# Kernel optimization log

Hardware: AMD Instinct MI355X
Metric: run time of the kernel (lower is better)

The kernel has to match this reference:

```python
import jax, jax.numpy as jnp
import numpy as np

B_SCALE = 1.3195079565048218  # per_level_scale
N_LEVELS = 4                  # kernel hardcodes 4 levels
F = 4                         # kernel hardcodes 4 features per level
BASE = 32.0                   # kernel hardcodes base resolution 32
MAX_PARAMS = 2 ** 19
N_POINTS = 2097152


def _level_meta():
    offsets = []
    off = 0
    for i in range(N_LEVELS):
        res = int(np.ceil(BASE * np.exp(i * np.log(B_SCALE)) - 1.0)) + 1
        p = res ** 3
        p = p if p % 8 == 0 else ((p + 7) // 8) * 8
        p = min(MAX_PARAMS, p)
        offsets.append(off)
        off += p
    return offsets, off

OFFSETS, TOTAL_PARAMS = _level_meta()
TOTAL_HASH_SIZE = TOTAL_PARAMS * F  # 2772480


def setup_inputs() -> dict:
    key = jax.random.key(0)
    k1, k2 = jax.random.split(key)
    # scale to [0, 0.9) so all 8 corner indices stay inside each level's grid
    positions = jax.random.uniform(k1, (N_POINTS, 3), dtype=jnp.float32) * 0.9
    # original init: uniform(-1e-4, 1e-4); small random values
    table = jax.random.normal(k2, (TOTAL_HASH_SIZE,), dtype=jnp.float32) * 1e-4
    return {"positions": positions, "table": table}


def _encode(positions, table):
    tab = table.reshape(-1, F)  # [total_params, 4]
    n = positions.shape[0]
    outs = []
    for level in range(N_LEVELS):
        scale = BASE * (B_SCALE ** level) - 1.0
        res = int(np.ceil(scale)) + 1
        pos = positions * scale + 0.5            # [n,3]
        grid = jnp.floor(pos)
        frac = pos - grid                         # trilinear fractions
        grid = grid.astype(jnp.int32)
        acc = jnp.zeros((n, F), positions.dtype)
        for c in range(8):  # 8 corners of the cell
            w = jnp.ones((n,), positions.dtype)
            idx = jnp.zeros((n,), jnp.int32)
            stride = 1
            for d in range(3):
                if (c >> d) & 1:
                    coord = grid[:, d] + 1
                    w = w * frac[:, d]
                else:
                    coord = grid[:, d]
                    w = w * (1.0 - frac[:, d])
                idx = idx + coord * stride
                stride *= res
            acc = acc + w[:, None] * tab[OFFSETS[level] + idx]
        outs.append(acc)
    return jnp.concatenate(outs, axis=1)  # [n, 16]


def reference(positions, table):
    return _encode(positions, table)
```

## Files before the change

kernel.cpp:

```cpp
#include <hip/hip_runtime.h>
#include <math.h>


#define NBINS        512
#define BIN_SCALE    (8.0f / 0.9f)
#define SCAT_THREADS 512
#define PTS_PER_BLK  4096
#define SCAT_ITERS   (PTS_PER_BLK / SCAT_THREADS)
#define CAP          4608

#define ENC_THREADS  512
#define ENC_BPB      (CAP / ENC_THREADS)

#define D1 7
#define D2 9
#define D3 11
#define A1 0
#define A2 (A1 + D1*D1*D1)
#define A3 (A2 + D2*D2*D2)
#define LDS_TOT (A3 + D3*D3*D3)

typedef float vfloat4 __attribute__((ext_vector_type(4)));

__device__ __forceinline__ int bin_of(float x, float y, float z) {
    int bx = (int)(x * BIN_SCALE); bx = bx < 0 ? 0 : (bx > 7 ? 7 : bx);
    int by = (int)(y * BIN_SCALE); by = by < 0 ? 0 : (by > 7 ? 7 : by);
    int bz = (int)(z * BIN_SCALE); bz = bz < 0 ? 0 : (bz > 7 ? 7 : bz);
    return bx | (by << 3) | (bz << 6);
}


__global__ __launch_bounds__(SCAT_THREADS) void scatter_cap_kernel(
    const float* __restrict__ pos, int n, int* __restrict__ cursor,
    float4* __restrict__ sorted, int bin_stride)
{
    __shared__ float4         lds_rec[PTS_PER_BLK];
    __shared__ unsigned short lds_bin[PTS_PER_BLK];
    __shared__ int lds_hist[NBINS];
    __shared__ int lds_lbase[NBINS];
    __shared__ int lds_gbase[NBINS];

    int tid = threadIdx.x;
    long base = (long)blockIdx.x * PTS_PER_BLK;
    lds_hist[tid] = 0;
    __syncthreads();

    float px[SCAT_ITERS], py[SCAT_ITERS], pz[SCAT_ITERS];
    int br[SCAT_ITERS];
#pragma unroll
    for (int j = 0; j < SCAT_ITERS; ++j) {
        long p = base + j * SCAT_THREADS + tid;
        int packed = -1;
        if (p < n) {
            float x = pos[3 * p], y = pos[3 * p + 1], z = pos[3 * p + 2];
            px[j] = x; py[j] = y; pz[j] = z;
            int b = bin_of(x, y, z);
            int r = atomicAdd(&lds_hist[b], 1);
            packed = (r << 9) | b;
        }
        br[j] = packed;
    }
    __syncthreads();

    int cntb = lds_hist[tid];
    lds_lbase[tid] = cntb;
    __syncthreads();
    for (int off = 1; off < NBINS; off <<= 1) {
        int v = (tid >= off) ? lds_lbase[tid - off] : 0;
        __syncthreads();
        lds_lbase[tid] += v;
        __syncthreads();
    }
    int excl = lds_lbase[tid] - cntb;
    if (cntb) lds_gbase[tid] = atomicAdd(&cursor[tid], cntb);
    lds_lbase[tid] = excl;
    __syncthreads();

#pragma unroll
    for (int j = 0; j < SCAT_ITERS; ++j) {
        if (br[j] < 0) continue;
        int b = br[j] & (NBINS - 1);
        int r = br[j] >> 9;
        int s = lds_lbase[b] + r;
        long p = base + j * SCAT_THREADS + tid;
        lds_rec[s] = make_float4(px[j], py[j], pz[j], __int_as_float((int)p));
        lds_bin[s] = (unsigned short)b;
    }
    __syncthreads();

    long rem = (long)n - base;
    int tot = rem >= PTS_PER_BLK ? PTS_PER_BLK : (rem > 0 ? (int)rem : 0);
    for (int s = tid; s < tot; s += SCAT_THREADS) {
        float4 rec = lds_rec[s];
        int b = lds_bin[s];
        int off_in_bin = s - lds_lbase[b];
        long slot = (long)b * bin_stride + lds_gbase[b] + off_in_bin;
        sorted[slot] = rec;
    }
}

template<int D>
__device__ __forceinline__ void stage_win(
    float4* __restrict__ dst, const float4* __restrict__ tab,
    int off, int res, int Bx, int By, int Bz, int tid)
{
    const int DD = D * D, DDD = D * D * D;
    for (int e = tid; e < DDD; e += ENC_THREADS) {
        int iz  = e / DD;
        int rem = e - iz * DD;
        int iy  = rem / D;
        int ix  = rem - iy * D;
        int gx = Bx + ix; gx = gx < 0 ? 0 : (gx > res - 1 ? res - 1 : gx);
        int gy = By + iy; gy = gy < 0 ? 0 : (gy > res - 1 ? res - 1 : gy);
        int gz = Bz + iz; gz = gz < 0 ? 0 : (gz > res - 1 ? res - 1 : gz);
        dst[e] = tab[off + gx + gy * res + gz * res * res];
    }
}

__device__ __forceinline__ float4 interp_global(
    const float4* __restrict__ tab,
    float x, float y, float z, float scale, int res, int off)
{
    float hx = x * scale + 0.5f, hy = y * scale + 0.5f, hz = z * scale + 0.5f;
    float fx = floorf(hx), fy = floorf(hy), fz = floorf(hz);
    float wx = hx - fx, wy = hy - fy, wz = hz - fz;
    float ox = 1.0f - wx, oy = 1.0f - wy, oz = 1.0f - wz;
    int res2  = res * res;
    int basei = off + (int)fx + (int)fy * res + (int)fz * res2;
    float4 acc = make_float4(0.f, 0.f, 0.f, 0.f);
#pragma unroll
    for (int c = 0; c < 8; ++c) {
        int   idx = basei + ((c & 1) ? 1 : 0) + ((c & 2) ? res : 0) + ((c & 4) ? res2 : 0);
        float w   = ((c & 1) ? wx : ox) * ((c & 2) ? wy : oy) * ((c & 4) ? wz : oz);
        float4 v  = tab[idx];
        acc.x += w * v.x; acc.y += w * v.y; acc.z += w * v.z; acc.w += w * v.w;
    }
    return acc;
}

template<int D>
__device__ __forceinline__ float4 interp_one(
    const float4* __restrict__ lds, const float4* __restrict__ tab,
    float x, float y, float z, float scale, int res, int off,
    int Bx, int By, int Bz)
{
    float hx = x * scale + 0.5f, hy = y * scale + 0.5f, hz = z * scale + 0.5f;
    float fx = floorf(hx), fy = floorf(hy), fz = floorf(hz);
    float wx = hx - fx, wy = hy - fy, wz = hz - fz;
    float ox = 1.0f - wx, oy = 1.0f - wy, oz = 1.0f - wz;
    int gx = (int)fx, gy = (int)fy, gz = (int)fz;
    int lx = gx - Bx, ly = gy - By, lz = gz - Bz;
    float4 acc = make_float4(0.f, 0.f, 0.f, 0.f);
    if ((unsigned)lx <= (unsigned)(D - 2) &&
        (unsigned)ly <= (unsigned)(D - 2) &&
        (unsigned)lz <= (unsigned)(D - 2)) {
        int basei = (lz * D + ly) * D + lx;
#pragma unroll
        for (int c = 0; c < 8; ++c) {
            int   idx = basei + ((c & 1) ? 1 : 0) + ((c & 2) ? D : 0) + ((c & 4) ? D * D : 0);
            float w   = ((c & 1) ? wx : ox) * ((c & 2) ? wy : oy) * ((c & 4) ? wz : oz);
            float4 v  = lds[idx];
            acc.x += w * v.x; acc.y += w * v.y; acc.z += w * v.z; acc.w += w * v.w;
        }
    } else {
        int res2  = res * res;
        int basei = off + gx + gy * res + gz * res2;
#pragma unroll
        for (int c = 0; c < 8; ++c) {
            int   idx = basei + ((c & 1) ? 1 : 0) + ((c & 2) ? res : 0) + ((c & 4) ? res2 : 0);
            float w   = ((c & 1) ? wx : ox) * ((c & 2) ? wy : oy) * ((c & 4) ? wz : oz);
            float4 v  = tab[idx];
            acc.x += w * v.x; acc.y += w * v.y; acc.z += w * v.z; acc.w += w * v.w;
        }
    }
    return acc;
}

__global__ __launch_bounds__(ENC_THREADS) void encode_cap_lds_kernel(
    const float4* __restrict__ sorted,
    const int* __restrict__ cursor,
    const float4* __restrict__ tab,
    float4* __restrict__ out,
    float s0, float s1, float s2, float s3,
    int r0, int r1, int r2, int r3,
    int o0, int o1, int o2, int o3)
{
    __shared__ float4 lds[LDS_TOT];

    int nb = (int)gridDim.x;
    int lb = (int)blockIdx.x;
    lb = (lb & 7) * (nb >> 3) + (lb >> 3);

    int b   = lb / ENC_BPB;
    int k   = lb - b * ENC_BPB;
    int cnt = cursor[b];
    if (k * ENC_THREADS >= cnt) return;

    int tid = threadIdx.x;

    int local = k * ENC_THREADS + tid;
    int j = b * CAP + local;
    vfloat4 rv = __builtin_nontemporal_load((const vfloat4*)&sorted[j]);

    int bx = b & 7, by = (b >> 3) & 7, bz = b >> 6;
    float lox = bx * 0.1125f, loy = by * 0.1125f, loz = bz * 0.1125f;

    int B1x = (int)floorf(lox * s1 + 0.5f), B1y = (int)floorf(loy * s1 + 0.5f), B1z = (int)floorf(loz * s1 + 0.5f);
    int B2x = (int)floorf(lox * s2 + 0.5f), B2y = (int)floorf(loy * s2 + 0.5f), B2z = (int)floorf(loz * s2 + 0.5f);
    int B3x = (int)floorf(lox * s3 + 0.5f), B3y = (int)floorf(loy * s3 + 0.5f), B3z = (int)floorf(loz * s3 + 0.5f);

    stage_win<D1>(lds + A1, tab, o1, r1, B1x, B1y, B1z, tid);
    stage_win<D2>(lds + A2, tab, o2, r2, B2x, B2y, B2z, tid);
    stage_win<D3>(lds + A3, tab, o3, r3, B3x, B3y, B3z, tid);
    __syncthreads();

    if (local >= cnt) return;

    float x = rv.x, y = rv.y, z = rv.z;
    int p = __float_as_int(rv.w);
    float4* op = out + (long)p * 4;

    float4 a0 = interp_global(tab, x, y, z, s0, r0, o0);
    op[0] = a0;
    float4 a1 = interp_one<D1>(lds + A1, tab, x, y, z, s1, r1, o1, B1x, B1y, B1z);
    op[1] = a1;
    float4 a2 = interp_one<D2>(lds + A2, tab, x, y, z, s2, r2, o2, B2x, B2y, B2z);
    op[2] = a2;
    float4 a3 = interp_one<D3>(lds + A3, tab, x, y, z, s3, r3, o3, B3x, B3y, B3z);
    op[3] = a3;
}


__device__ __forceinline__ void interp_levels(
    float4 rec, const float4* __restrict__ tab, float4* __restrict__ o,
    float s0, float s1, float s2, float s3,
    int r0, int r1, int r2, int r3,
    int o0, int o1, int o2, int o3)
{
    float scales[4] = { s0, s1, s2, s3 };
    int   ress[4]   = { r0, r1, r2, r3 };
    int   offs[4]   = { o0, o1, o2, o3 };
#pragma unroll
    for (int l = 0; l < 4; ++l) {
        float scale = scales[l];
        int   res   = ress[l];
        int   off   = offs[l];
        float hx = rec.x * scale + 0.5f;
        float hy = rec.y * scale + 0.5f;
        float hz = rec.z * scale + 0.5f;
        float gx = floorf(hx), gy = floorf(hy), gz = floorf(hz);
        float wx = hx - gx,   wy = hy - gy,   wz = hz - gz;
        float ox = 1.0f - wx, oy = 1.0f - wy, oz = 1.0f - wz;
        int res2 = res * res;
        int base = off + (int)gx + (int)gy * res + (int)gz * res2;
        float4 acc = make_float4(0.f, 0.f, 0.f, 0.f);
#pragma unroll
        for (int c = 0; c < 8; ++c) {
            int   idx = base + ((c & 1) ? 1 : 0) + ((c & 2) ? res : 0) + ((c & 4) ? res2 : 0);
            float w   = ((c & 1) ? wx : ox) * ((c & 2) ? wy : oy) * ((c & 4) ? wz : oz);
            float4 v  = tab[idx];
            acc.x += w * v.x; acc.y += w * v.y; acc.z += w * v.z; acc.w += w * v.w;
        }
        o[l] = acc;
    }
}


__global__ __launch_bounds__(SCAT_THREADS) void hist_kernel(
    const float* __restrict__ pos, int n, int* __restrict__ hist)
{
    __shared__ int lh[NBINS];
    int tid = threadIdx.x;
    lh[tid] = 0;
    __syncthreads();
    long base = (long)blockIdx.x * PTS_PER_BLK;
#pragma unroll
    for (int j = 0; j < SCAT_ITERS; ++j) {
        long p = base + j * SCAT_THREADS + tid;
        if (p < n) {
            float x = pos[3 * p], y = pos[3 * p + 1], z = pos[3 * p + 2];
            atomicAdd(&lh[bin_of(x, y, z)], 1);
        }
    }
    __syncthreads();
    int c = lh[tid];
    if (c) atomicAdd(&hist[tid], c);
}

__global__ __launch_bounds__(256) void scan_kernel(
    const int* __restrict__ hist, int* __restrict__ cursor)
{
    __shared__ int partials[256];
    int t = threadIdx.x;
    int a = hist[2 * t], b = hist[2 * t + 1];
    int sum = a + b;
    partials[t] = sum;
    __syncthreads();
    for (int off = 1; off < 256; off <<= 1) {
        int v = (t >= off) ? partials[t - off] : 0;
        __syncthreads();
        partials[t] += v;
        __syncthreads();
    }
    int base = partials[t] - sum;
    cursor[2 * t]     = base;
    cursor[2 * t + 1] = base + a;
}

__global__ __launch_bounds__(256) void encode_kernel(
    const float4* __restrict__ sorted, const float4* __restrict__ tab,
    float4* __restrict__ out, int n,
    float s0, float s1, float s2, float s3,
    int r0, int r1, int r2, int r3,
    int o0, int o1, int o2, int o3)
{
    int j = blockIdx.x * blockDim.x + threadIdx.x;
    if (j >= n) return;
    vfloat4 rv = __builtin_nontemporal_load((const vfloat4*)&sorted[j]);
    float4 rec = make_float4(rv.x, rv.y, rv.z, rv.w);
    int p = __float_as_int(rec.w);
    interp_levels(rec, tab, out + (long)p * 4,
                  s0, s1, s2, s3, r0, r1, r2, r3, o0, o1, o2, o3);
}

__global__ __launch_bounds__(256) void encode_direct_kernel(
    const float* __restrict__ pos, const float4* __restrict__ tab,
    float4* __restrict__ out, int n_points,
    float s0, float s1, float s2, float s3,
    int r0, int r1, int r2, int r3,
    int o0, int o1, int o2, int o3)
{
    int t = blockIdx.x * blockDim.x + threadIdx.x;
    int p = t >> 2;
    if (p >= n_points) return;
    int l = t & 3;
    float scale = (l == 0) ? s0 : (l == 1) ? s1 : (l == 2) ? s2 : s3;
    int   res   = (l == 0) ? r0 : (l == 1) ? r1 : (l == 2) ? r2 : r3;
    int   off   = (l == 0) ? o0 : (l == 1) ? o1 : (l == 2) ? o2 : o3;
    float px = pos[3 * p], py = pos[3 * p + 1], pz = pos[3 * p + 2];
    float hx = px * scale + 0.5f, hy = py * scale + 0.5f, hz = pz * scale + 0.5f;
    float gx = floorf(hx), gy = floorf(hy), gz = floorf(hz);
    float wx = hx - gx, wy = hy - gy, wz = hz - gz;
    float ox = 1.f - wx, oy = 1.f - wy, oz = 1.f - wz;
    int res2 = res * res;
    int base = off + (int)gx + (int)gy * res + (int)gz * res2;
    float4 acc = make_float4(0.f, 0.f, 0.f, 0.f);
#pragma unroll
    for (int c = 0; c < 8; ++c) {
        int   idx = base + ((c & 1) ? 1 : 0) + ((c & 2) ? res : 0) + ((c & 4) ? res2 : 0);
        float w   = ((c & 1) ? wx : ox) * ((c & 2) ? wy : oy) * ((c & 4) ? wz : oz);
        float4 v  = tab[idx];
        acc.x += w * v.x; acc.y += w * v.y; acc.z += w * v.z; acc.w += w * v.w;
    }
    out[t] = acc;
}

extern "C" void kernel_launch(void* const* d_in, const int* in_sizes, int n_in,
                              void* d_out, int out_size, void* d_ws, size_t ws_size,
                              hipStream_t stream) {
    const float*  positions = (const float*)d_in[0];
    const float4* table     = (const float4*)d_in[1];
    float4*       out       = (float4*)d_out;
    int n = in_sizes[0] / 3;

    const double B_SCALE = 1.3195079565048218;
    const double BASE = 32.0;
    const long   MAX_PARAMS = 1L << 19;
    float scales[4]; int res[4], offs[4];
    long off = 0;
    for (int l = 0; l < 4; ++l) {
        double s = BASE * pow(B_SCALE, (double)l) - 1.0;
        scales[l] = (float)s;
        int r = (int)ceil(s) + 1;
        res[l] = r;
        offs[l] = (int)off;
        long pcount = (long)r * r * r;
        if (pcount % 8 != 0) pcount = (pcount + 7) / 8 * 8;
        if (pcount > MAX_PARAMS) pcount = MAX_PARAMS;
        off += pcount;
    }

    size_t need_cap   = (size_t)NBINS * sizeof(int) + (size_t)NBINS * CAP * 16;
    size_t need_exact = (size_t)NBINS * sizeof(int) * 2 + (size_t)n * 16;

    if (ws_size >= need_cap && n <= NBINS * (CAP - 512)) {
        int*    cursor = (int*)d_ws;
        float4* sorted = (float4*)(cursor + NBINS);

        int grid_pts = (n + PTS_PER_BLK - 1) / PTS_PER_BLK;
        int grid_enc = NBINS * ENC_BPB;

        (void)hipMemsetAsync(cursor, 0, NBINS * sizeof(int), stream);
        scatter_cap_kernel<<<grid_pts, SCAT_THREADS, 0, stream>>>(
            positions, n, cursor, sorted, CAP);
        encode_cap_lds_kernel<<<grid_enc, ENC_THREADS, 0, stream>>>(
            sorted, cursor, table, out,
            scales[0], scales[1], scales[2], scales[3],
            res[0], res[1], res[2], res[3],
            offs[0], offs[1], offs[2], offs[3]);
    } else if (ws_size >= need_exact) {
        int*    hist   = (int*)d_ws;
        int*    cursor = hist + NBINS;
        float4* sorted = (float4*)(cursor + NBINS);

        int grid_pts = (n + PTS_PER_BLK - 1) / PTS_PER_BLK;
        int grid_enc = (n + 255) / 256;

        (void)hipMemsetAsync(hist, 0, NBINS * sizeof(int), stream);
        hist_kernel<<<grid_pts, SCAT_THREADS, 0, stream>>>(positions, n, hist);
        scan_kernel<<<1, 256, 0, stream>>>(hist, cursor);
        scatter_cap_kernel<<<grid_pts, SCAT_THREADS, 0, stream>>>(
            positions, n, cursor, sorted, 0);
        encode_kernel<<<grid_enc, 256, 0, stream>>>(
            sorted, table, out, n,
            scales[0], scales[1], scales[2], scales[3],
            res[0], res[1], res[2], res[3],
            offs[0], offs[1], offs[2], offs[3]);
    } else {
        long n_threads = 4L * n;
        long grid = (n_threads + 255) / 256;
        encode_direct_kernel<<<dim3((unsigned)grid), dim3(256), 0, stream>>>(
            positions, table, out, n,
            scales[0], scales[1], scales[2], scales[3],
            res[0], res[1], res[2], res[3],
            offs[0], offs[1], offs[2], offs[3]);
    }
}
```

Measured before the change: 242.0 us.

## Prefetch level-0 corners before LDS staging; coalesce scatter input loads and shuffle scan

```diff
diff --git a/kernel.cpp b/kernel.cpp
--- a/kernel.cpp
+++ b/kernel.cpp
@@ -5,7 +5,7 @@
 #define NBINS        512
 #define BIN_SCALE    (8.0f / 0.9f)
 #define SCAT_THREADS 512
-#define PTS_PER_BLK  4096
+#define PTS_PER_BLK  2048
 #define SCAT_ITERS   (PTS_PER_BLK / SCAT_THREADS)
 #define CAP          4608
 
@@ -39,20 +39,33 @@
     __shared__ int lds_hist[NBINS];
     __shared__ int lds_lbase[NBINS];
     __shared__ int lds_gbase[NBINS];
+    __shared__ int lds_wsum[8];
 
     int tid = threadIdx.x;
     long base = (long)blockIdx.x * PTS_PER_BLK;
     lds_hist[tid] = 0;
+
+    long rem = (long)n - base;
+    int tot = rem >= PTS_PER_BLK ? PTS_PER_BLK : (rem > 0 ? (int)rem : 0);
+
+    float* fbuf = (float*)lds_rec;
+    int nflt = 3 * tot;
+    int nf4  = nflt >> 2;
+    const float4* posv = (const float4*)(pos + base * 3);
+    for (int f = tid; f < nf4; f += SCAT_THREADS)
+        ((float4*)fbuf)[f] = posv[f];
+    for (int q = (nf4 << 2) + tid; q < nflt; q += SCAT_THREADS)
+        fbuf[q] = pos[base * 3 + q];
     __syncthreads();
 
     float px[SCAT_ITERS], py[SCAT_ITERS], pz[SCAT_ITERS];
     int br[SCAT_ITERS];
 #pragma unroll
     for (int j = 0; j < SCAT_ITERS; ++j) {
-        long p = base + j * SCAT_THREADS + tid;
+        int lp = j * SCAT_THREADS + tid;
         int packed = -1;
-        if (p < n) {
-            float x = pos[3 * p], y = pos[3 * p + 1], z = pos[3 * p + 2];
+        if (lp < tot) {
+            float x = fbuf[3 * lp], y = fbuf[3 * lp + 1], z = fbuf[3 * lp + 2];
             px[j] = x; py[j] = y; pz[j] = z;
             int b = bin_of(x, y, z);
             int r = atomicAdd(&lds_hist[b], 1);
@@ -62,17 +75,29 @@
     }
     __syncthreads();
 
+    int lane = tid & 63, wid = tid >> 6;
     int cntb = lds_hist[tid];
-    lds_lbase[tid] = cntb;
-    __syncthreads();
-    for (int off = 1; off < NBINS; off <<= 1) {
-        int v = (tid >= off) ? lds_lbase[tid - off] : 0;
-        __syncthreads();
-        lds_lbase[tid] += v;
-        __syncthreads();
-    }
-    int excl = lds_lbase[tid] - cntb;
+    int v = cntb;
+#pragma unroll
+    for (int off = 1; off < 64; off <<= 1) {
+        int u = __shfl_up(v, off, 64);
+        if (lane >= off) v += u;
+    }
+    if (lane == 63) lds_wsum[wid] = v;
+    __syncthreads();
+    if (tid < 8) {
+        int w = lds_wsum[tid];
+#pragma unroll
+        for (int off = 1; off < 8; off <<= 1) {
+            int u = __shfl_up(w, off, 8);
+            if (tid >= off) w += u;
+        }
+        lds_wsum[tid] = w;
+    }
     if (cntb) lds_gbase[tid] = atomicAdd(&cursor[tid], cntb);
+    __syncthreads();
+    int wbase = wid ? lds_wsum[wid - 1] : 0;
+    int excl  = wbase + v - cntb;
     lds_lbase[tid] = excl;
     __syncthreads();
 
@@ -82,14 +107,12 @@
         int b = br[j] & (NBINS - 1);
         int r = br[j] >> 9;
         int s = lds_lbase[b] + r;
-        long p = base + j * SCAT_THREADS + tid;
-        lds_rec[s] = make_float4(px[j], py[j], pz[j], __int_as_float((int)p));
+        int lp = j * SCAT_THREADS + tid;
+        lds_rec[s] = make_float4(px[j], py[j], pz[j], __int_as_float((int)(base + lp)));
         lds_bin[s] = (unsigned short)b;
     }
     __syncthreads();
 
-    long rem = (long)n - base;
-    int tot = rem >= PTS_PER_BLK ? PTS_PER_BLK : (rem > 0 ? (int)rem : 0);
     for (int s = tid; s < tot; s += SCAT_THREADS) {
         float4 rec = lds_rec[s];
         int b = lds_bin[s];
@@ -115,27 +138,6 @@
         int gz = Bz + iz; gz = gz < 0 ? 0 : (gz > res - 1 ? res - 1 : gz);
         dst[e] = tab[off + gx + gy * res + gz * res * res];
     }
-}
-
-__device__ __forceinline__ float4 interp_global(
-    const float4* __restrict__ tab,
-    float x, float y, float z, float scale, int res, int off)
-{
-    float hx = x * scale + 0.5f, hy = y * scale + 0.5f, hz = z * scale + 0.5f;
-    float fx = floorf(hx), fy = floorf(hy), fz = floorf(hz);
-    float wx = hx - fx, wy = hy - fy, wz = hz - fz;
-    float ox = 1.0f - wx, oy = 1.0f - wy, oz = 1.0f - wz;
-    int res2  = res * res;
-    int basei = off + (int)fx + (int)fy * res + (int)fz * res2;
-    float4 acc = make_float4(0.f, 0.f, 0.f, 0.f);
-#pragma unroll
-    for (int c = 0; c < 8; ++c) {
-        int   idx = basei + ((c & 1) ? 1 : 0) + ((c & 2) ? res : 0) + ((c & 4) ? res2 : 0);
-        float w   = ((c & 1) ? wx : ox) * ((c & 2) ? wy : oy) * ((c & 4) ? wz : oz);
-        float4 v  = tab[idx];
-        acc.x += w * v.x; acc.y += w * v.y; acc.z += w * v.z; acc.w += w * v.w;
-    }
-    return acc;
 }
 
 template<int D>
@@ -202,6 +204,19 @@
     int j = b * CAP + local;
     vfloat4 rv = __builtin_nontemporal_load((const vfloat4*)&sorted[j]);
 
+    float hx0 = rv.x * s0 + 0.5f, hy0 = rv.y * s0 + 0.5f, hz0 = rv.z * s0 + 0.5f;
+    float fx0 = floorf(hx0), fy0 = floorf(hy0), fz0 = floorf(hz0);
+    float wx0 = hx0 - fx0, wy0 = hy0 - fy0, wz0 = hz0 - fz0;
+    int gx0 = (int)fx0; gx0 = gx0 < 0 ? 0 : (gx0 > r0 - 2 ? r0 - 2 : gx0);
+    int gy0 = (int)fy0; gy0 = gy0 < 0 ? 0 : (gy0 > r0 - 2 ? r0 - 2 : gy0);
+    int gz0 = (int)fz0; gz0 = gz0 < 0 ? 0 : (gz0 > r0 - 2 ? r0 - 2 : gz0);
+    int res20 = r0 * r0;
+    int base0 = o0 + gx0 + gy0 * r0 + gz0 * res20;
+    float4 L0[8];
+#pragma unroll
+    for (int c = 0; c < 8; ++c)
+        L0[c] = tab[base0 + ((c & 1) ? 1 : 0) + ((c & 2) ? r0 : 0) + ((c & 4) ? res20 : 0)];
+
     int bx = b & 7, by = (b >> 3) & 7, bz = b >> 6;
     float lox = bx * 0.1125f, loy = by * 0.1125f, loz = bz * 0.1125f;
 
@@ -220,8 +235,17 @@
     int p = __float_as_int(rv.w);
     float4* op = out + (long)p * 4;
 
-    float4 a0 = interp_global(tab, x, y, z, s0, r0, o0);
-    op[0] = a0;
+    {
+        float ox0 = 1.0f - wx0, oy0 = 1.0f - wy0, oz0 = 1.0f - wz0;
+        float4 acc = make_float4(0.f, 0.f, 0.f, 0.f);
+#pragma unroll
+        for (int c = 0; c < 8; ++c) {
+            float w = ((c & 1) ? wx0 : ox0) * ((c & 2) ? wy0 : oy0) * ((c & 4) ? wz0 : oz0);
+            acc.x += w * L0[c].x; acc.y += w * L0[c].y;
+            acc.z += w * L0[c].z; acc.w += w * L0[c].w;
+        }
+        op[0] = acc;
+    }
     float4 a1 = interp_one<D1>(lds + A1, tab, x, y, z, s1, r1, o1, B1x, B1y, B1z);
     op[1] = a1;
     float4 a2 = interp_one<D2>(lds + A2, tab, x, y, z, s2, r2, o2, B2x, B2y, B2z);
```

After: 252.9 us. 4.5% more time.

## Use one block per bin, stage level-0 window in LDS, prefetch points

Applied to the files above, without the earlier changes.

```diff
diff --git a/kernel.cpp b/kernel.cpp
--- a/kernel.cpp
+++ b/kernel.cpp
@@ -9,13 +9,14 @@
 #define SCAT_ITERS   (PTS_PER_BLK / SCAT_THREADS)
 #define CAP          4608
 
-#define ENC_THREADS  512
-#define ENC_BPB      (CAP / ENC_THREADS)
-
+#define ENC_THREADS  1024
+
+#define D0 6
 #define D1 7
 #define D2 9
 #define D3 11
-#define A1 0
+#define A0 0
+#define A1 (A0 + D0*D0*D0)
 #define A2 (A1 + D1*D1*D1)
 #define A3 (A2 + D2*D2*D2)
 #define LDS_TOT (A3 + D3*D3*D3)
@@ -115,27 +116,6 @@
         int gz = Bz + iz; gz = gz < 0 ? 0 : (gz > res - 1 ? res - 1 : gz);
         dst[e] = tab[off + gx + gy * res + gz * res * res];
     }
-}
-
-__device__ __forceinline__ float4 interp_global(
-    const float4* __restrict__ tab,
-    float x, float y, float z, float scale, int res, int off)
-{
-    float hx = x * scale + 0.5f, hy = y * scale + 0.5f, hz = z * scale + 0.5f;
-    float fx = floorf(hx), fy = floorf(hy), fz = floorf(hz);
-    float wx = hx - fx, wy = hy - fy, wz = hz - fz;
-    float ox = 1.0f - wx, oy = 1.0f - wy, oz = 1.0f - wz;
-    int res2  = res * res;
-    int basei = off + (int)fx + (int)fy * res + (int)fz * res2;
-    float4 acc = make_float4(0.f, 0.f, 0.f, 0.f);
-#pragma unroll
-    for (int c = 0; c < 8; ++c) {
-        int   idx = basei + ((c & 1) ? 1 : 0) + ((c & 2) ? res : 0) + ((c & 4) ? res2 : 0);
-        float w   = ((c & 1) ? wx : ox) * ((c & 2) ? wy : oy) * ((c & 4) ? wz : oz);
-        float4 v  = tab[idx];
-        acc.x += w * v.x; acc.y += w * v.y; acc.z += w * v.z; acc.w += w * v.w;
-    }
-    return acc;
 }
 
 template<int D>
@@ -176,7 +156,7 @@
     return acc;
 }
 
-__global__ __launch_bounds__(ENC_THREADS) void encode_cap_lds_kernel(
+__global__ __launch_bounds__(ENC_THREADS) void encode_bin_kernel(
     const float4* __restrict__ sorted,
     const int* __restrict__ cursor,
     const float4* __restrict__ tab,
@@ -188,46 +168,55 @@
     __shared__ float4 lds[LDS_TOT];
 
     int nb = (int)gridDim.x;
-    int lb = (int)blockIdx.x;
-    lb = (lb & 7) * (nb >> 3) + (lb >> 3);
-
-    int b   = lb / ENC_BPB;
-    int k   = lb - b * ENC_BPB;
+    int b  = (int)blockIdx.x;
+    b = (b & 7) * (nb >> 3) + (b >> 3);
+
     int cnt = cursor[b];
-    if (k * ENC_THREADS >= cnt) return;
-
     int tid = threadIdx.x;
-
-    int local = k * ENC_THREADS + tid;
-    int j = b * CAP + local;
-    vfloat4 rv = __builtin_nontemporal_load((const vfloat4*)&sorted[j]);
 
     int bx = b & 7, by = (b >> 3) & 7, bz = b >> 6;
     float lox = bx * 0.1125f, loy = by * 0.1125f, loz = bz * 0.1125f;
 
+    int B0x = (int)floorf(lox * s0 + 0.5f), B0y = (int)floorf(loy * s0 + 0.5f), B0z = (int)floorf(loz * s0 + 0.5f);
     int B1x = (int)floorf(lox * s1 + 0.5f), B1y = (int)floorf(loy * s1 + 0.5f), B1z = (int)floorf(loz * s1 + 0.5f);
     int B2x = (int)floorf(lox * s2 + 0.5f), B2y = (int)floorf(loy * s2 + 0.5f), B2z = (int)floorf(loz * s2 + 0.5f);
     int B3x = (int)floorf(lox * s3 + 0.5f), B3y = (int)floorf(loy * s3 + 0.5f), B3z = (int)floorf(loz * s3 + 0.5f);
 
+    stage_win<D0>(lds + A0, tab, o0, r0, B0x, B0y, B0z, tid);
     stage_win<D1>(lds + A1, tab, o1, r1, B1x, B1y, B1z, tid);
     stage_win<D2>(lds + A2, tab, o2, r2, B2x, B2y, B2z, tid);
     stage_win<D3>(lds + A3, tab, o3, r3, B3x, B3y, B3z, tid);
     __syncthreads();
 
-    if (local >= cnt) return;
-
-    float x = rv.x, y = rv.y, z = rv.z;
-    int p = __float_as_int(rv.w);
-    float4* op = out + (long)p * 4;
-
-    float4 a0 = interp_global(tab, x, y, z, s0, r0, o0);
-    op[0] = a0;
-    float4 a1 = interp_one<D1>(lds + A1, tab, x, y, z, s1, r1, o1, B1x, B1y, B1z);
-    op[1] = a1;
-    float4 a2 = interp_one<D2>(lds + A2, tab, x, y, z, s2, r2, o2, B2x, B2y, B2z);
-    op[2] = a2;
-    float4 a3 = interp_one<D3>(lds + A3, tab, x, y, z, s3, r3, o3, B3x, B3y, B3z);
-    op[3] = a3;
+    if (cnt == 0) return;
+
+    int iters = (cnt + ENC_THREADS - 1) / ENC_THREADS;
+    const float4* sbin = sorted + (long)b * CAP;
+    int jmax = CAP - 1;
+
+    int local = tid;
+    vfloat4 rv = __builtin_nontemporal_load(
+        (const vfloat4*)&sbin[local <= jmax ? local : jmax]);
+
+    for (int it = 0; it < iters; ++it) {
+        int nloc = local + ENC_THREADS;
+        vfloat4 nx = rv;
+        if (it + 1 < iters)
+            nx = __builtin_nontemporal_load(
+                (const vfloat4*)&sbin[nloc <= jmax ? nloc : jmax]);
+        if (local < cnt) {
+            float x = rv.x, y = rv.y, z = rv.z;
+            int p = __float_as_int(rv.w);
+            float4* op = out + (long)p * 4;
+            float4 a0 = interp_one<D0>(lds + A0, tab, x, y, z, s0, r0, o0, B0x, B0y, B0z);
+            float4 a1 = interp_one<D1>(lds + A1, tab, x, y, z, s1, r1, o1, B1x, B1y, B1z);
+            float4 a2 = interp_one<D2>(lds + A2, tab, x, y, z, s2, r2, o2, B2x, B2y, B2z);
+            float4 a3 = interp_one<D3>(lds + A3, tab, x, y, z, s3, r3, o3, B3x, B3y, B3z);
+            op[0] = a0; op[1] = a1; op[2] = a2; op[3] = a3;
+        }
+        rv = nx;
+        local = nloc;
+    }
 }
 
 
@@ -388,12 +377,11 @@
         float4* sorted = (float4*)(cursor + NBINS);
 
         int grid_pts = (n + PTS_PER_BLK - 1) / PTS_PER_BLK;
-        int grid_enc = NBINS * ENC_BPB;
 
         (void)hipMemsetAsync(cursor, 0, NBINS * sizeof(int), stream);
         scatter_cap_kernel<<<grid_pts, SCAT_THREADS, 0, stream>>>(
             positions, n, cursor, sorted, CAP);
-        encode_cap_lds_kernel<<<grid_enc, ENC_THREADS, 0, stream>>>(
+        encode_bin_kernel<<<NBINS, ENC_THREADS, 0, stream>>>(
             sorted, cursor, table, out,
             scales[0], scales[1], scales[2], scales[3],
             res[0], res[1], res[2], res[3],
```

Measured after the change: 228.6 us. 5.5% less time.
